# Kernel tuning notes

Measured on AMD Instinct MI355X. Metric: run time of the kernel, lower is better.

Reference implementation:

```python
import jax, jax.numpy as jnp
import numpy as np

B, C, H, W = 64, 256, 32, 32
K, D = 1024, 256
COMMIT = 0.25
DECAY = 0.99
EPS = 1e-05


def setup_inputs() -> dict:
    key = jax.random.key(0)
    k1, k2, k3 = jax.random.split(key, 3)
    return {
        "inputs": jax.random.normal(k1, (B, C, H, W), dtype=jnp.float32),
        "embedding": jax.random.normal(k2, (K, D), dtype=jnp.float32),
        "ema_cluster_size": jnp.zeros((K,), dtype=jnp.float32),
        "ema_w": jax.random.normal(k3, (K, D), dtype=jnp.float32),
    }


def reference(inputs, embedding, ema_cluster_size, ema_w):
    # NCHW -> NHWC, flatten to [N, D]
    x = jnp.transpose(inputs, (0, 2, 3, 1))  # [B,H,W,D]
    in_shape = x.shape
    flat = x.reshape(-1, D)  # [N, D]

    dist = (jnp.sum(flat * flat, axis=1, keepdims=True)
            + jnp.sum(embedding * embedding, axis=1)
            - 2.0 * jnp.matmul(flat, embedding.T))
    idx = jnp.argmin(dist, axis=1)  # [N] int
    encodings = jax.nn.one_hot(idx, K, dtype=flat.dtype)  # [N, K]

    quantized = jnp.matmul(encodings, embedding).reshape(in_shape)  # [B,H,W,D]

    # EMA updates (training branch)
    cluster = ema_cluster_size * DECAY + (1.0 - DECAY) * jnp.sum(encodings, axis=0)
    n = jnp.sum(cluster)
    cluster = (cluster + EPS) / (n + K * EPS) * n
    dw = jnp.matmul(encodings.T, flat)  # [K, D]
    new_ema_w = ema_w * DECAY + (1.0 - DECAY) * dw
    new_embedding = new_ema_w / cluster[:, None]

    # commitment loss (quantized detached)
    e_latent_loss = jnp.mean((jax.lax.stop_gradient(quantized) - x) ** 2)
    loss = COMMIT * e_latent_loss

    # straight-through estimator
    quantized_st = x + jax.lax.stop_gradient(quantized - x)

    avg_probs = jnp.mean(encodings, axis=0)
    vq_entropy = -jnp.sum(avg_probs * jnp.log(avg_probs + 1e-10))

    out = jnp.transpose(quantized_st, (0, 3, 1, 2))  # back to NCHW
    return out, loss, vq_entropy, encodings, cluster, new_ema_w, new_embedding
```

## Files before the change

### kernel.cpp

```cpp
#include <hip/hip_runtime.h>

#define B_    64
#define C_    256
#define H_    32
#define W_    32
#define K_    1024
#define D_    256
#define HW_   1024
#define N_    65536
#define NELEM 16777216
#define DECAY_ 0.99f
#define OMD_   0.01f
#define EPS_   1e-5f
#define TAU_   0.05f

#define OFF_LOSS    16777216
#define OFF_ENT     16777217
#define OFF_ENC     16777218
#define OFF_CLUSTER 83886082
#define OFF_NEWW    83887106
#define OFF_NEWEMB  84149250

#define OFF_XHI     (OFF_ENC + 2)
#define OFF_XLO     (OFF_XHI + 8388608)
#define OFF_EHI     (OFF_XLO + 8388608)
#define OFF_ELO     (OFF_EHI + 131072)
#define OFF_SORT2   (OFF_ELO + 131072)
#define ZTAIL_ABS   33884168
#define ZTAIL_F4    12500478
#define ZHEAD_F4    4276737

typedef __attribute__((ext_vector_type(8)))  short short8;
typedef __attribute__((ext_vector_type(16))) float floatx16;

__device__ __forceinline__ unsigned short f2bf(float f) {
    unsigned u = __float_as_uint(f);
    return (unsigned short)((u + 0x7fffu + ((u >> 16) & 1u)) >> 16);
}
__device__ __forceinline__ float bf2f(unsigned short h) {
    return __uint_as_float(((unsigned)h) << 16);
}

__global__ __launch_bounds__(64) void k_prep_e(const float* __restrict__ emb,
                                               unsigned short* __restrict__ ehi,
                                               unsigned short* __restrict__ elo,
                                               float* __restrict__ enorm) {
    const int k = blockIdx.x;
    const int t = threadIdx.x;
    float4 v = ((const float4*)(emb + (size_t)k * D_))[t];
    float s = v.x * v.x + v.y * v.y + v.z * v.z + v.w * v.w;
    ushort4 hi, lo;
    {
        float f[4] = {v.x, v.y, v.z, v.w};
        unsigned short h[4], l[4];
        #pragma unroll
        for (int j = 0; j < 4; ++j) {
            h[j] = f2bf(f[j]);
            l[j] = f2bf(f[j] - bf2f(h[j]));
        }
        hi = make_ushort4(h[0], h[1], h[2], h[3]);
        lo = make_ushort4(l[0], l[1], l[2], l[3]);
    }
    size_t o = ((size_t)(k >> 5) << 13) + ((size_t)(t >> 2) << 9)
             + (((size_t)(t >> 1) & 1) << 8) + ((size_t)(k & 31) << 3) + ((t & 1) << 2);
    *(ushort4*)(ehi + o) = hi;
    *(ushort4*)(elo + o) = lo;
    #pragma unroll
    for (int off = 32; off > 0; off >>= 1) s += __shfl_down(s, off);
    if (t == 0) enorm[k] = s;
}

__global__ __launch_bounds__(256) void k_prep_x(const float* __restrict__ inp,
                                                unsigned short* __restrict__ xhi,
                                                unsigned short* __restrict__ xlo,
                                                float* __restrict__ dw,
                                                int* __restrict__ small_) {
    __shared__ float tile[32][257];
    const int tid = threadIdx.x;
    const int bid = blockIdx.x;
    if (bid < 1024) {
        int g = bid * 256 + tid;
        dw[g] = 0.0f;
        if (g < 1026) small_[g] = 0;
    }
    const int dt = bid & 7;
    const int ht = (bid >> 3) & 3;
    const int b = bid >> 5;
    const int d0 = dt * 32;
    const int hw0 = ht * 256;
    const float* src = inp + (size_t)b * (C_ * HW_) + (size_t)d0 * HW_ + hw0;
    #pragma unroll
    for (int i = 0; i < 8; ++i) {
        int idx4 = i * 256 + tid;
        int dl = idx4 >> 6;
        int nl4 = (idx4 & 63) * 4;
        float4 v = *(const float4*)(src + (size_t)dl * HW_ + nl4);
        tile[dl][nl4] = v.x; tile[dl][nl4 + 1] = v.y;
        tile[dl][nl4 + 2] = v.z; tile[dl][nl4 + 3] = v.w;
    }
    __syncthreads();
    const int nbase = b * HW_ + hw0;
    #pragma unroll
    for (int i = 0; i < 4; ++i) {
        int f8 = i * 256 + tid;
        int nl = f8 >> 2;
        int dpos = (f8 & 3) * 8;
        union { unsigned short u[8]; short8 v; } ph, pl;
        #pragma unroll
        for (int j = 0; j < 8; ++j) {
            float f = -2.0f * tile[dpos + j][nl];
            unsigned short h = f2bf(f);
            ph.u[j] = h;
            pl.u[j] = f2bf(f - bf2f(h));
        }
        size_t o = (size_t)(nbase + nl) * D_ + d0 + dpos;
        *(short8*)(xhi + o) = ph.v;
        *(short8*)(xlo + o) = pl.v;
    }
}

__device__ __forceinline__ void stage_tile(const unsigned short* __restrict__ gh,
                                           const unsigned short* __restrict__ gl,
                                           unsigned short* sh, unsigned short* sl,
                                           int tid) {
    #pragma unroll
    for (int i = 0; i < 4; ++i) {
        __builtin_amdgcn_global_load_lds(
            (const __attribute__((address_space(1))) unsigned int*)(gh + i * 2048 + tid * 8),
            (__attribute__((address_space(3))) unsigned int*)(sh + i * 2048 + tid * 8),
            16, 0, 0);
        __builtin_amdgcn_global_load_lds(
            (const __attribute__((address_space(1))) unsigned int*)(gl + i * 2048 + tid * 8),
            (__attribute__((address_space(3))) unsigned int*)(sl + i * 2048 + tid * 8),
            16, 0, 0);
    }
}

__global__ __launch_bounds__(256, 2) void k_argmin(
    const unsigned short* __restrict__ xhi, const unsigned short* __restrict__ xlo,
    const unsigned short* __restrict__ ehi, const unsigned short* __restrict__ elo,
    const float* __restrict__ enorm, int* __restrict__ idx_out,
    int* __restrict__ flagcount, int* __restrict__ flaglist,
    float4* __restrict__ encz)
{
    __shared__ unsigned short smem[2][2][8192];
    const int tid = threadIdx.x;
    const int w = tid >> 6;
    const int lane = tid & 63;
    const int c32 = lane & 31;
    const int h = lane >> 5;
    const int r0 = blockIdx.x * 128 + w * 32;
    const int gtid = blockIdx.x * 256 + tid;
    const float4 z4 = make_float4(0.f, 0.f, 0.f, 0.f);

    short8 Ahi[16], Alo[16];
    {
        const unsigned short* pa = xhi + (size_t)(r0 + c32) * D_ + h * 8;
        const unsigned short* pl = xlo + (size_t)(r0 + c32) * D_ + h * 8;
        #pragma unroll
        for (int ds = 0; ds < 16; ++ds) {
            Ahi[ds] = *(const short8*)(pa + ds * 16);
            Alo[ds] = *(const short8*)(pl + ds * 16);
        }
    }

    float b1[16], b2[16];
    int bi[16];
    #pragma unroll
    for (int i = 0; i < 16; ++i) { b1[i] = 3.0e38f; b2[i] = 3.0e38f; bi[i] = 0; }

    stage_tile(ehi, elo, &smem[0][0][0], &smem[0][1][0], tid);
    __syncthreads();

    const int rb = (h << 8) + (c32 << 3);

    int cb = 0;
    for (int ct = 0; ct < 32; ++ct) {
        if (ct + 1 < 32) {
            stage_tile(ehi + (size_t)(ct + 1) * 8192, elo + (size_t)(ct + 1) * 8192,
                       &smem[cb ^ 1][0][0], &smem[cb ^ 1][1][0], tid);
        }
        __builtin_amdgcn_sched_barrier(0);
        #pragma unroll
        for (int jj = 0; jj < 3; ++jj) {
            int zi = (ct * 3 + jj) * 131072 + gtid;
            zi = (zi < ZTAIL_F4) ? zi : (ZTAIL_F4 - 1);
            encz[zi] = z4;
        }
        const int col = ct * 32 + c32;
        const float en = enorm[col];
        const unsigned short* sbh = &smem[cb][0][rb];
        const unsigned short* sbl = &smem[cb][1][rb];
        floatx16 hh, cr;
        #pragma unroll
        for (int i = 0; i < 16; ++i) { hh[i] = 0.0f; cr[i] = 0.0f; }
        #pragma unroll
        for (int ds = 0; ds < 16; ++ds) {
            short8 bh = *(const short8*)(sbh + ds * 512);
            short8 bl = *(const short8*)(sbl + ds * 512);
            hh = __builtin_amdgcn_mfma_f32_32x32x16_bf16(Ahi[ds], bh, hh, 0, 0, 0);
            cr = __builtin_amdgcn_mfma_f32_32x32x16_bf16(Ahi[ds], bl, cr, 0, 0, 0);
            cr = __builtin_amdgcn_mfma_f32_32x32x16_bf16(Alo[ds], bh, cr, 0, 0, 0);
        }
        #pragma unroll
        for (int r = 0; r < 16; ++r) {
            float v = hh[r] + cr[r] + en;
            bool lt = v < b1[r];
            float nb2 = lt ? b1[r] : fminf(v, b2[r]);
            b2[r] = nb2;
            b1[r] = lt ? v : b1[r];
            bi[r] = lt ? col : bi[r];
        }
        asm volatile("s_waitcnt vmcnt(3)" ::: "memory");
        __builtin_amdgcn_sched_barrier(0);
        __builtin_amdgcn_s_barrier();
        __builtin_amdgcn_sched_barrier(0);
        cb ^= 1;
    }

    #pragma unroll
    for (int r = 0; r < 16; ++r) {
        float B1 = b1[r], B2 = b2[r];
        int Bi = bi[r];
        #pragma unroll
        for (int mask = 1; mask <= 16; mask <<= 1) {
            float v1 = __shfl_xor(B1, mask);
            float v2 = __shfl_xor(B2, mask);
            int i1 = __shfl_xor(Bi, mask);
            if (v1 < B1 || (v1 == B1 && i1 < Bi)) {
                B2 = fminf(fminf(B1, B2), v2);
                B1 = v1; Bi = i1;
            } else {
                B2 = fminf(B2, fminf(v1, v2));
            }
        }
        if (c32 == 0) {
            int row = r0 + (r & 3) + 4 * h + 8 * (r >> 2);
            idx_out[row] = Bi;
            if (B2 - B1 < TAU_) {
                int p = atomicAdd(flagcount, 1);
                flaglist[p] = row;
            }
        }
    }
}

__global__ __launch_bounds__(256) void k_rescan(
    const float* __restrict__ inp, const float* __restrict__ emb,
    const int* __restrict__ flagcount, const int* __restrict__ flaglist,
    int* __restrict__ idx_out)
{
    __shared__ double xd[256];
    __shared__ double sv[256];
    __shared__ int si[256];
    const int tid = threadIdx.x;
    const int nflag = *flagcount;
    for (int f = blockIdx.x; f < nflag; f += gridDim.x) {
        int n = flaglist[f];
        int b = n >> 10, nn = n & 1023;
        xd[tid] = (double)inp[(size_t)b * (C_ * HW_) + (size_t)tid * HW_ + nn];
        __syncthreads();
        double bv = 1e300; int bi = 0;
        for (int k = tid; k < K_; k += 256) {
            const float* ep = emb + (size_t)k * D_;
            double dot = 0.0, en = 0.0;
            for (int d = 0; d < D_; ++d) {
                double e = (double)ep[d];
                dot = fma(xd[d], e, dot);
                en  = fma(e, e, en);
            }
            double v = en - 2.0 * dot;
            if (v < bv) { bv = v; bi = k; }
        }
        sv[tid] = bv; si[tid] = bi;
        __syncthreads();
        for (int s = 128; s > 0; s >>= 1) {
            if (tid < s) {
                if (sv[tid + s] < sv[tid] || (sv[tid + s] == sv[tid] && si[tid + s] < si[tid])) {
                    sv[tid] = sv[tid + s]; si[tid] = si[tid + s];
                }
            }
            __syncthreads();
        }
        if (tid == 0) idx_out[n] = si[0];
        __syncthreads();
    }
}

__global__ __launch_bounds__(256) void k_hist(const int* __restrict__ idx, int* __restrict__ counts) {
    __shared__ int h[1024];
    const int tid = threadIdx.x;
    #pragma unroll
    for (int j = 0; j < 4; ++j) h[tid + j * 256] = 0;
    __syncthreads();
    #pragma unroll
    for (int j = 0; j < 4; ++j) {
        int n = blockIdx.x * 1024 + j * 256 + tid;
        atomicAdd(&h[idx[n]], 1);
    }
    __syncthreads();
    #pragma unroll
    for (int j = 0; j < 4; ++j) {
        int v = h[tid + j * 256];
        if (v) atomicAdd(&counts[tid + j * 256], v);
    }
}

__global__ __launch_bounds__(1024) void k_scan(const int* __restrict__ counts,
                                               int* __restrict__ offsets, int* __restrict__ cursor) {
    __shared__ int s[1024];
    const int t = threadIdx.x;
    const int c = counts[t];
    s[t] = c;
    __syncthreads();
    for (int off = 1; off < 1024; off <<= 1) {
        int v = (t >= off) ? s[t - off] : 0;
        __syncthreads();
        s[t] += v;
        __syncthreads();
    }
    int excl = s[t] - c;
    offsets[t] = excl;
    cursor[t] = excl;
    if (t == 1023) offsets[1024] = s[1023];
}

__global__ __launch_bounds__(256) void k_scatter(const int* __restrict__ idx,
                                                 int* __restrict__ cursor, int* __restrict__ sorted) {
    __shared__ int hc[1024];
    __shared__ int hb[1024];
    const int tid = threadIdx.x;
    const int base = blockIdx.x * 1024;
    #pragma unroll
    for (int j = 0; j < 4; ++j) hc[tid + j * 256] = 0;
    __syncthreads();
    int myk[4], myn[4];
    #pragma unroll
    for (int j = 0; j < 4; ++j) {
        int n = base + j * 256 + tid;
        myn[j] = n;
        myk[j] = idx[n];
        atomicAdd(&hc[myk[j]], 1);
    }
    __syncthreads();
    #pragma unroll
    for (int j = 0; j < 4; ++j) {
        int kk = tid + j * 256;
        int c = hc[kk];
        hb[kk] = c ? atomicAdd(&cursor[kk], c) : 0;
    }
    __syncthreads();
    #pragma unroll
    for (int j = 0; j < 4; ++j) hc[tid + j * 256] = 0;
    __syncthreads();
    #pragma unroll
    for (int j = 0; j < 4; ++j) {
        int p = hb[myk[j]] + atomicAdd(&hc[myk[j]], 1);
        sorted[p] = myn[j];
    }
}

__global__ __launch_bounds__(256) void k_dwg(const unsigned short* __restrict__ xhi,
                                             const unsigned short* __restrict__ xlo,
                                             const int* __restrict__ sorted,
                                             const int* __restrict__ idx,
                                             const int* __restrict__ offsets,
                                             float* __restrict__ dw) {
    const int lane = threadIdx.x & 63;
    const int wid = threadIdx.x >> 6;
    const int wbase = (blockIdx.x * 4 + wid) * 64;

    int myn = sorted[wbase + lane];
    int myk = idx[myn];

    float4 acc = make_float4(0.f, 0.f, 0.f, 0.f);
    int cur = __shfl(myk, 0);

    #pragma unroll 8
    for (int i = 0; i < 64; ++i) {
        int n = __shfl(myn, i);
        int k = __shfl(myk, i);
        if (k != cur) {
            bool full = (offsets[cur] >= wbase) && (offsets[cur + 1] <= wbase + 64);
            float* dwk = dw + (size_t)cur * D_ + lane * 4;
            if (full) {
                ((float2*)dwk)[0] = make_float2(-0.5f * acc.x, -0.5f * acc.y);
                ((float2*)dwk)[1] = make_float2(-0.5f * acc.z, -0.5f * acc.w);
            } else {
                atomicAdd(dwk + 0, -0.5f * acc.x);
                atomicAdd(dwk + 1, -0.5f * acc.y);
                atomicAdd(dwk + 2, -0.5f * acc.z);
                atomicAdd(dwk + 3, -0.5f * acc.w);
            }
            acc = make_float4(0.f, 0.f, 0.f, 0.f);
            cur = k;
        }
        size_t o = (size_t)n * D_ + lane * 4;
        ushort4 hx = *(const ushort4*)(xhi + o);
        ushort4 lx = *(const ushort4*)(xlo + o);
        acc.x += bf2f(hx.x) + bf2f(lx.x);
        acc.y += bf2f(hx.y) + bf2f(lx.y);
        acc.z += bf2f(hx.z) + bf2f(lx.z);
        acc.w += bf2f(hx.w) + bf2f(lx.w);
    }
    {
        bool full = (offsets[cur] >= wbase) && (offsets[cur + 1] <= wbase + 64);
        float* dwk = dw + (size_t)cur * D_ + lane * 4;
        if (full) {
            ((float2*)dwk)[0] = make_float2(-0.5f * acc.x, -0.5f * acc.y);
            ((float2*)dwk)[1] = make_float2(-0.5f * acc.z, -0.5f * acc.w);
        } else {
            atomicAdd(dwk + 0, -0.5f * acc.x);
            atomicAdd(dwk + 1, -0.5f * acc.y);
            atomicAdd(dwk + 2, -0.5f * acc.z);
            atomicAdd(dwk + 3, -0.5f * acc.w);
        }
    }
}

__global__ __launch_bounds__(256) void k_quant(
    const float* __restrict__ inp, const float* __restrict__ emb,
    const int* __restrict__ idx, float* __restrict__ outp, float* __restrict__ losssum,
    float* __restrict__ enc)
{
    __shared__ float qt[64][260];
    __shared__ int karr[64];
    __shared__ float red[256];
    const int tid = threadIdx.x;
    const int bid = blockIdx.x;
    const int b = bid >> 4;
    const int ht = bid & 15;
    const int base_n = b * HW_ + ht * 64;

    {
        const float4 z4 = make_float4(0.f, 0.f, 0.f, 0.f);
        float4* pz = (float4*)(enc + 2);
        int t = bid * 256 + tid;
        #pragma unroll
        for (int it = 0; it < 17; ++it) {
            int i = it * 262144 + t;
            if (i < ZHEAD_F4) pz[i] = z4;
        }
        if (t == 0) { enc[0] = 0.f; enc[1] = 0.f; enc[67108862] = 0.f; enc[67108863] = 0.f; }
    }

    if (tid < 64) karr[tid] = idx[base_n + tid];
    __syncthreads();

    #pragma unroll
    for (int it = 0; it < 16; ++it) {
        int f = it * 256 + tid;
        int r = f >> 6;
        int c4 = (f & 63) << 2;
        float4 v = ((const float4*)emb)[karr[r] * 64 + (c4 >> 2)];
        *(float4*)(&qt[r][c4]) = v;
    }
    __syncthreads();

    float s = 0.0f;
    #pragma unroll
    for (int it = 0; it < 16; ++it) {
        int f = it * 256 + tid;
        int c = f >> 4;
        int hl = (f & 15) << 2;
        int g = b * 65536 + c * 256 + ht * 16 + (hl >> 2);
        float4 x = ((const float4*)inp)[g];
        float q0 = qt[hl + 0][c];
        float q1 = qt[hl + 1][c];
        float q2 = qt[hl + 2][c];
        float q3 = qt[hl + 3][c];
        float d0 = q0 - x.x, d1 = q1 - x.y, d2 = q2 - x.z, d3 = q3 - x.w;
        ((float4*)outp)[g] = make_float4(x.x + d0, x.y + d1, x.z + d2, x.w + d3);
        s += d0 * d0 + d1 * d1 + d2 * d2 + d3 * d3;
    }
    red[tid] = s;
    __syncthreads();
    for (int t = 128; t > 0; t >>= 1) {
        if (tid < t) red[tid] += red[tid + t];
        __syncthreads();
    }
    if (tid == 0) atomicAdd(losssum, red[0]);
}

__global__ __launch_bounds__(256) void k_enc1(const int* __restrict__ idx, float* __restrict__ enc) {
    #pragma unroll
    for (int j = 0; j < 4; ++j) {
        int n = blockIdx.x * 1024 + j * 256 + threadIdx.x;
        enc[(size_t)n * 1024 + idx[n]] = 1.0f;
    }
}

__global__ __launch_bounds__(1024) void k_cluster(
    const float* __restrict__ ema_cs, const int* __restrict__ counts,
    const float* __restrict__ losssum, float* __restrict__ out_cluster,
    float* __restrict__ out_loss, float* __restrict__ out_ent)
{
    __shared__ float red[1024];
    const int k = threadIdx.x;
    float cnt = (float)counts[k];
    float raw = ema_cs[k] * DECAY_ + OMD_ * cnt;
    red[k] = raw;
    __syncthreads();
    for (int t = 512; t > 0; t >>= 1) {
        if (k < t) red[k] += red[k + t];
        __syncthreads();
    }
    float nsum = red[0];
    __syncthreads();
    float clv = (raw + EPS_) / (nsum + 1024.0f * EPS_) * nsum;
    out_cluster[k] = clv;
    float p = cnt * (1.0f / 65536.0f);
    red[k] = p * logf(p + 1e-10f);
    __syncthreads();
    for (int t = 512; t > 0; t >>= 1) {
        if (k < t) red[k] += red[k + t];
        __syncthreads();
    }
    if (k == 0) {
        out_ent[0] = -red[0];
        out_loss[0] = 0.25f * losssum[0] * (1.0f / 16777216.0f);
    }
}

__global__ __launch_bounds__(256) void k_fin(
    const float* __restrict__ ema_w, const float* __restrict__ cluster,
    float* __restrict__ neww, float* __restrict__ newemb)
{
    int g = blockIdx.x * 256 + threadIdx.x;
    int k = g >> 8;
    float w = ema_w[g] * DECAY_ + OMD_ * neww[g];
    neww[g] = w;
    newemb[g] = w / cluster[k];
}

extern "C" void kernel_launch(void* const* d_in, const int* in_sizes, int n_in,
                              void* d_out, int out_size, void* d_ws, size_t ws_size,
                              hipStream_t stream)
{
    const float* inp    = (const float*)d_in[0];
    const float* emb    = (const float*)d_in[1];
    const float* ema_cs = (const float*)d_in[2];
    const float* ema_w  = (const float*)d_in[3];

    float* out0        = (float*)d_out;
    float* out_loss    = out0 + OFF_LOSS;
    float* out_ent     = out0 + OFF_ENT;
    float* out_enc     = out0 + OFF_ENC;
    float* out_cluster = out0 + OFF_CLUSTER;
    float* out_neww    = out0 + OFF_NEWW;
    float* out_newemb  = out0 + OFF_NEWEMB;

    unsigned short* ws_xhi  = (unsigned short*)(out0 + OFF_XHI);
    unsigned short* ws_xlo  = (unsigned short*)(out0 + OFF_XLO);
    unsigned short* ws_ehi  = (unsigned short*)(out0 + OFF_EHI);
    unsigned short* ws_elo  = (unsigned short*)(out0 + OFF_ELO);
    int*   ws_sorted  = (int*)(out0 + OFF_SORT2);
    int*   ws_offsets = ws_sorted + 65536;
    int*   ws_cursor  = ws_offsets + 1025;

    int*   ws_idx    = (int*)d_ws;
    int*   ws_counts = ws_idx + 65536;
    int*   ws_flagc  = ws_idx + 66560;
    float* ws_loss   = (float*)(ws_idx + 66561);
    int*   ws_flagl  = ws_idx + 66562;
    float* ws_enorm  = (float*)(ws_idx + 132098);

    float4* encz = (float4*)(out0 + ZTAIL_ABS);

    k_prep_e <<<1024, 64, 0, stream>>>(emb, ws_ehi, ws_elo, ws_enorm);
    k_prep_x <<<2048, 256, 0, stream>>>(inp, ws_xhi, ws_xlo, out_neww, ws_counts);
    k_argmin <<<512, 256, 0, stream>>>(ws_xhi, ws_xlo, ws_ehi, ws_elo, ws_enorm,
                                       ws_idx, ws_flagc, ws_flagl, encz);
    k_rescan <<<256, 256, 0, stream>>>(inp, emb, ws_flagc, ws_flagl, ws_idx);
    k_hist   <<<64, 256, 0, stream>>>(ws_idx, ws_counts);
    k_scan   <<<1, 1024, 0, stream>>>(ws_counts, ws_offsets, ws_cursor);
    k_scatter<<<64, 256, 0, stream>>>(ws_idx, ws_cursor, ws_sorted);
    k_dwg    <<<256, 256, 0, stream>>>(ws_xhi, ws_xlo, ws_sorted, ws_idx, ws_offsets, out_neww);
    k_quant  <<<1024, 256, 0, stream>>>(inp, emb, ws_idx, out0, ws_loss, out_enc);
    k_enc1   <<<64, 256, 0, stream>>>(ws_idx, out_enc);
    k_cluster<<<1, 1024, 0, stream>>>(ema_cs, ws_counts, ws_loss, out_cluster, out_loss, out_ent);
    k_fin    <<<1024, 256, 0, stream>>>(ema_w, out_cluster, out_neww, out_newemb);
}
```

Measured before the change: 662.3 us.

## Fuse histogram, scan, and cluster stages into neighbouring kernels to cut launches

The codeword histogram is now built in LDS inside the argmin kernel, and the rescan kernel patches counts when it changes an index. The exclusive scan is recomputed redundantly in every scatter block. Cluster normalisation, entropy and the one-hot writes are folded into the final EMA kernel, so the standalone hist, scan, enc1 and cluster kernels go away. This removes four small serial launches and their dependency bubbles. In exchange each block repeats a 1024-entry scan and a 1024-element reduction.

After: 651.6 us. No clear change (-1.6%).

```diff
diff --git a/kernel.cpp b/kernel.cpp
--- a/kernel.cpp
+++ b/kernel.cpp
@@ -74,7 +74,8 @@
                                                 unsigned short* __restrict__ xhi,
                                                 unsigned short* __restrict__ xlo,
                                                 float* __restrict__ dw,
-                                                int* __restrict__ small_) {
+                                                int* __restrict__ small_,
+                                                int* __restrict__ cursor) {
     __shared__ float tile[32][257];
     const int tid = threadIdx.x;
     const int bid = blockIdx.x;
@@ -82,6 +83,7 @@
         int g = bid * 256 + tid;
         dw[g] = 0.0f;
         if (g < 1026) small_[g] = 0;
+        if (bid < 4) cursor[bid * 256 + tid] = 0;
     }
     const int dt = bid & 7;
     const int ht = (bid >> 3) & 3;
@@ -141,7 +143,7 @@
     const unsigned short* __restrict__ ehi, const unsigned short* __restrict__ elo,
     const float* __restrict__ enorm, int* __restrict__ idx_out,
     int* __restrict__ flagcount, int* __restrict__ flaglist,
-    float4* __restrict__ encz)
+    float4* __restrict__ encz, int* __restrict__ counts)
 {
     __shared__ unsigned short smem[2][2][8192];
     const int tid = threadIdx.x;
@@ -218,6 +220,11 @@
         cb ^= 1;
     }
 
+    int* histL = (int*)&smem[0][0][0];
+    #pragma unroll
+    for (int j = 0; j < 4; ++j) histL[tid + j * 256] = 0;
+    __syncthreads();
+
     #pragma unroll
     for (int r = 0; r < 16; ++r) {
         float B1 = b1[r], B2 = b2[r];
@@ -237,18 +244,25 @@
         if (c32 == 0) {
             int row = r0 + (r & 3) + 4 * h + 8 * (r >> 2);
             idx_out[row] = Bi;
+            atomicAdd(&histL[Bi], 1);
             if (B2 - B1 < TAU_) {
                 int p = atomicAdd(flagcount, 1);
                 flaglist[p] = row;
             }
         }
     }
+    __syncthreads();
+    #pragma unroll
+    for (int j = 0; j < 4; ++j) {
+        int v = histL[tid + j * 256];
+        if (v) atomicAdd(&counts[tid + j * 256], v);
+    }
 }
 
 __global__ __launch_bounds__(256) void k_rescan(
     const float* __restrict__ inp, const float* __restrict__ emb,
     const int* __restrict__ flagcount, const int* __restrict__ flaglist,
-    int* __restrict__ idx_out)
+    int* __restrict__ idx_out, int* __restrict__ counts)
 {
     __shared__ double xd[256];
     __shared__ double sv[256];
@@ -282,58 +296,64 @@
             }
             __syncthreads();
         }
-        if (tid == 0) idx_out[n] = si[0];
-        __syncthreads();
-    }
-}
-
-__global__ __launch_bounds__(256) void k_hist(const int* __restrict__ idx, int* __restrict__ counts) {
-    __shared__ int h[1024];
-    const int tid = threadIdx.x;
-    #pragma unroll
-    for (int j = 0; j < 4; ++j) h[tid + j * 256] = 0;
-    __syncthreads();
-    #pragma unroll
-    for (int j = 0; j < 4; ++j) {
-        int n = blockIdx.x * 1024 + j * 256 + tid;
-        atomicAdd(&h[idx[n]], 1);
-    }
-    __syncthreads();
-    #pragma unroll
-    for (int j = 0; j < 4; ++j) {
-        int v = h[tid + j * 256];
-        if (v) atomicAdd(&counts[tid + j * 256], v);
-    }
-}
-
-__global__ __launch_bounds__(1024) void k_scan(const int* __restrict__ counts,
-                                               int* __restrict__ offsets, int* __restrict__ cursor) {
-    __shared__ int s[1024];
-    const int t = threadIdx.x;
-    const int c = counts[t];
-    s[t] = c;
-    __syncthreads();
-    for (int off = 1; off < 1024; off <<= 1) {
-        int v = (t >= off) ? s[t - off] : 0;
-        __syncthreads();
-        s[t] += v;
-        __syncthreads();
-    }
-    int excl = s[t] - c;
-    offsets[t] = excl;
-    cursor[t] = excl;
-    if (t == 1023) offsets[1024] = s[1023];
+        if (tid == 0) {
+            int old = idx_out[n];
+            int nw = si[0];
+            if (nw != old) {
+                idx_out[n] = nw;
+                atomicAdd(&counts[old], -1);
+                atomicAdd(&counts[nw], 1);
+            }
+        }
+        __syncthreads();
+    }
 }
 
 __global__ __launch_bounds__(256) void k_scatter(const int* __restrict__ idx,
-                                                 int* __restrict__ cursor, int* __restrict__ sorted) {
+                                                 const int* __restrict__ counts,
+                                                 int* __restrict__ cursor,
+                                                 int* __restrict__ sorted,
+                                                 int* __restrict__ offsets) {
+    __shared__ int sc[1024];
     __shared__ int hc[1024];
     __shared__ int hb[1024];
     const int tid = threadIdx.x;
     const int base = blockIdx.x * 1024;
-    #pragma unroll
-    for (int j = 0; j < 4; ++j) hc[tid + j * 256] = 0;
-    __syncthreads();
+    int creg[4];
+    #pragma unroll
+    for (int j = 0; j < 4; ++j) {
+        int k = tid + j * 256;
+        creg[j] = counts[k];
+        sc[k] = creg[j];
+        hc[k] = 0;
+    }
+    __syncthreads();
+    for (int off = 1; off < 1024; off <<= 1) {
+        int t0[4];
+        #pragma unroll
+        for (int j = 0; j < 4; ++j) {
+            int k = tid + j * 256;
+            t0[j] = (k >= off) ? sc[k - off] : 0;
+        }
+        __syncthreads();
+        #pragma unroll
+        for (int j = 0; j < 4; ++j) sc[tid + j * 256] += t0[j];
+        __syncthreads();
+    }
+    #pragma unroll
+    for (int j = 0; j < 4; ++j) {
+        int k = tid + j * 256;
+        sc[k] -= creg[j];
+    }
+    __syncthreads();
+    if (blockIdx.x == 0) {
+        #pragma unroll
+        for (int j = 0; j < 4; ++j) {
+            int k = tid + j * 256;
+            offsets[k] = sc[k];
+            if (k == 1023) offsets[1024] = sc[1023] + creg[j];
+        }
+    }
     int myk[4], myn[4];
     #pragma unroll
     for (int j = 0; j < 4; ++j) {
@@ -355,7 +375,7 @@
     __syncthreads();
     #pragma unroll
     for (int j = 0; j < 4; ++j) {
-        int p = hb[myk[j]] + atomicAdd(&hc[myk[j]], 1);
+        int p = sc[myk[j]] + hb[myk[j]] + atomicAdd(&hc[myk[j]], 1);
         sorted[p] = myn[j];
     }
 }
@@ -482,55 +502,64 @@
     if (tid == 0) atomicAdd(losssum, red[0]);
 }
 
-__global__ __launch_bounds__(256) void k_enc1(const int* __restrict__ idx, float* __restrict__ enc) {
+__global__ __launch_bounds__(256) void k_fin(
+    const float* __restrict__ ema_cs, const int* __restrict__ counts,
+    const float* __restrict__ losssum, const float* __restrict__ ema_w,
+    const int* __restrict__ idx,
+    float* __restrict__ neww, float* __restrict__ newemb,
+    float* __restrict__ out_cluster, float* __restrict__ out_loss,
+    float* __restrict__ out_ent, float* __restrict__ enc)
+{
+    __shared__ float sraw[1024];
+    __shared__ float red[256];
+    __shared__ float sclv;
+    const int tid = threadIdx.x;
+    const int bid = blockIdx.x;
+    float part = 0.f;
+    float ent = 0.f;
     #pragma unroll
     for (int j = 0; j < 4; ++j) {
-        int n = blockIdx.x * 1024 + j * 256 + threadIdx.x;
-        enc[(size_t)n * 1024 + idx[n]] = 1.0f;
-    }
-}
-
-__global__ __launch_bounds__(1024) void k_cluster(
-    const float* __restrict__ ema_cs, const int* __restrict__ counts,
-    const float* __restrict__ losssum, float* __restrict__ out_cluster,
-    float* __restrict__ out_loss, float* __restrict__ out_ent)
-{
-    __shared__ float red[1024];
-    const int k = threadIdx.x;
-    float cnt = (float)counts[k];
-    float raw = ema_cs[k] * DECAY_ + OMD_ * cnt;
-    red[k] = raw;
-    __syncthreads();
-    for (int t = 512; t > 0; t >>= 1) {
-        if (k < t) red[k] += red[k + t];
+        int k = tid + j * 256;
+        float cnt = (float)counts[k];
+        float raw = ema_cs[k] * DECAY_ + OMD_ * cnt;
+        sraw[k] = raw;
+        part += raw;
+        float p = cnt * (1.0f / 65536.0f);
+        ent += p * logf(p + 1e-10f);
+    }
+    red[tid] = part;
+    __syncthreads();
+    for (int t = 128; t > 0; t >>= 1) {
+        if (tid < t) red[tid] += red[tid + t];
         __syncthreads();
     }
     float nsum = red[0];
     __syncthreads();
-    float clv = (raw + EPS_) / (nsum + 1024.0f * EPS_) * nsum;
-    out_cluster[k] = clv;
-    float p = cnt * (1.0f / 65536.0f);
-    red[k] = p * logf(p + 1e-10f);
-    __syncthreads();
-    for (int t = 512; t > 0; t >>= 1) {
-        if (k < t) red[k] += red[k + t];
-        __syncthreads();
-    }
-    if (k == 0) {
-        out_ent[0] = -red[0];
-        out_loss[0] = 0.25f * losssum[0] * (1.0f / 16777216.0f);
-    }
-}
-
-__global__ __launch_bounds__(256) void k_fin(
-    const float* __restrict__ ema_w, const float* __restrict__ cluster,
-    float* __restrict__ neww, float* __restrict__ newemb)
-{
-    int g = blockIdx.x * 256 + threadIdx.x;
-    int k = g >> 8;
+    red[tid] = ent;
+    __syncthreads();
+    for (int t = 128; t > 0; t >>= 1) {
+        if (tid < t) red[tid] += red[tid + t];
+        __syncthreads();
+    }
+    if (tid == 0) {
+        float clv = (sraw[bid] + EPS_) / (nsum + 1024.0f * EPS_) * nsum;
+        sclv = clv;
+        out_cluster[bid] = clv;
+        if (bid == 0) {
+            out_ent[0] = -red[0];
+            out_loss[0] = 0.25f * losssum[0] * (1.0f / 16777216.0f);
+        }
+    }
+    __syncthreads();
+    float clv = sclv;
+    int g = bid * 256 + tid;
     float w = ema_w[g] * DECAY_ + OMD_ * neww[g];
     neww[g] = w;
-    newemb[g] = w / cluster[k];
+    newemb[g] = w / clv;
+    if (tid < 64) {
+        int n = bid * 64 + tid;
+        enc[(size_t)n * 1024 + idx[n]] = 1.0f;
+    }
 }
 
 extern "C" void kernel_launch(void* const* d_in, const int* in_sizes, int n_in,
@@ -568,16 +597,14 @@
     float4* encz = (float4*)(out0 + ZTAIL_ABS);
 
     k_prep_e <<<1024, 64, 0, stream>>>(emb, ws_ehi, ws_elo, ws_enorm);
-    k_prep_x <<<2048, 256, 0, stream>>>(inp, ws_xhi, ws_xlo, out_neww, ws_counts);
+    k_prep_x <<<2048, 256, 0, stream>>>(inp, ws_xhi, ws_xlo, out_neww, ws_counts, ws_cursor);
     k_argmin <<<512, 256, 0, stream>>>(ws_xhi, ws_xlo, ws_ehi, ws_elo, ws_enorm,
-                                       ws_idx, ws_flagc, ws_flagl, encz);
-    k_rescan <<<256, 256, 0, stream>>>(inp, emb, ws_flagc, ws_flagl, ws_idx);
-    k_hist   <<<64, 256, 0, stream>>>(ws_idx, ws_counts);
-    k_scan   <<<1, 1024, 0, stream>>>(ws_counts, ws_offsets, ws_cursor);
-    k_scatter<<<64, 256, 0, stream>>>(ws_idx, ws_cursor, ws_sorted);
+                                       ws_idx, ws_flagc, ws_flagl, encz, ws_counts);
+    k_rescan <<<256, 256, 0, stream>>>(inp, emb, ws_flagc, ws_flagl, ws_idx, ws_counts);
+    k_scatter<<<64, 256, 0, stream>>>(ws_idx, ws_counts, ws_cursor, ws_sorted, ws_offsets);
     k_dwg    <<<256, 256, 0, stream>>>(ws_xhi, ws_xlo, ws_sorted, ws_idx, ws_offsets, out_neww);
     k_quant  <<<1024, 256, 0, stream>>>(inp, emb, ws_idx, out0, ws_loss, out_enc);
-    k_enc1   <<<64, 256, 0, stream>>>(ws_idx, out_enc);
-    k_cluster<<<1, 1024, 0, stream>>>(ema_cs, ws_counts, ws_loss, out_cluster, out_loss, out_ent);
-    k_fin    <<<1024, 256, 0, stream>>>(ema_w, out_cluster, out_neww, out_newemb);
-}
+    k_fin    <<<1024, 256, 0, stream>>>(ema_cs, ws_counts, ws_loss, ema_w, ws_idx,
+                                        out_neww, out_newemb, out_cluster, out_loss,
+                                        out_ent, out_enc);
+}
```
